# Optimization experiments

Hardware: AMD Instinct MI355X
Metric: run time of the kernel (lower is better)

## Reference

```python
import jax, jax.numpy as jnp
import numpy as np


def setup_inputs() -> dict:
    key = jax.random.key(0)
    k1, k2, k3, k4 = jax.random.split(key, 4)
    N, E, F_IN, F_OUT = 50000, 800000, 128, 128
    x = jax.random.normal(k1, (N, F_IN), dtype=jnp.float32)
    src = jax.random.randint(k2, (E,), 0, N, dtype=jnp.int32)
    dst = jax.random.randint(k3, (E,), 0, N, dtype=jnp.int32)
    # Linear(2*in, out, bias=False) weight, torch layout (out, 2*in)
    W = jax.random.normal(k4, (F_OUT, 2 * F_IN), dtype=jnp.float32) * (1.0 / np.sqrt(2 * F_IN))
    return {"x": x, "src": src, "dst": dst, "num_nodes": N, "W": W}


def reference(x, src, dst, num_nodes, W):
    # Mean aggregation over sparse adjacency (edge list src -> dst):
    # aggregated[v] = mean_{u in N(v)} x[u]
    msgs = x[src]                                            # [E, F] gather
    summed = jax.ops.segment_sum(msgs, dst, num_segments=num_nodes)  # [N, F]
    deg = jax.ops.segment_sum(jnp.ones_like(dst, dtype=x.dtype), dst,
                              num_segments=num_nodes)        # [N]
    agg = summed / jnp.maximum(deg, 1.0)[:, None]            # mean, safe for isolated nodes
    h = jnp.concatenate([x, agg], axis=1)                    # [N, 2F]
    out = h @ W.T                                            # [N, F_out]
    return jax.nn.relu(out)
```

## Files before the change

### kernel.cpp

```cpp
#include <hip/hip_runtime.h>
#include <hip/hip_bf16.h>

typedef __attribute__((ext_vector_type(8))) short short8;
typedef __attribute__((ext_vector_type(4))) float f32x4;

#define BKS      6
#define BKN      64
#define ITERA    16
#define NBMAX    1024
#define CAPB_MAX 3072

__device__ __forceinline__ unsigned short f2bf(float f) {
    unsigned u = __builtin_bit_cast(unsigned, f);
    u += 0x7fffu + ((u >> 16) & 1u);
    return (unsigned short)(u >> 16);
}
__device__ __forceinline__ float bf2f(unsigned short b) {
    return __builtin_bit_cast(float, ((unsigned)b) << 16);
}

__global__ void prep_kernel(const float* __restrict__ x,
                            unsigned short* __restrict__ xb,
                            const float* __restrict__ W,
                            unsigned short* __restrict__ Wp,
                            unsigned* __restrict__ gcur, int nb, int nx8) {
    int i = blockIdx.x * blockDim.x + threadIdx.x;
    if (i < nx8) {
        const float4* p = (const float4*)(x + (size_t)i * 8);
        float4 lo = p[0], hi = p[1];
        short8 v;
        v[0] = (short)f2bf(lo.x); v[1] = (short)f2bf(lo.y);
        v[2] = (short)f2bf(lo.z); v[3] = (short)f2bf(lo.w);
        v[4] = (short)f2bf(hi.x); v[5] = (short)f2bf(hi.y);
        v[6] = (short)f2bf(hi.z); v[7] = (short)f2bf(hi.w);
        *(short8*)(xb + (size_t)i * 8) = v;
    }
    if (i < 4096) {
        const float4* p = (const float4*)(W + (size_t)i * 8);
        float4 lo = p[0], hi = p[1];
        short8 v;
        v[0] = (short)f2bf(lo.x); v[1] = (short)f2bf(lo.y);
        v[2] = (short)f2bf(lo.z); v[3] = (short)f2bf(lo.w);
        v[4] = (short)f2bf(hi.x); v[5] = (short)f2bf(hi.y);
        v[6] = (short)f2bf(hi.z); v[7] = (short)f2bf(hi.w);
        int r    = i >> 5;
        int c0   = (i & 31) << 3;
        int ct   = r >> 4;
        int arow = r & 15;
        int ks   = c0 >> 5;
        int kgrp = (c0 >> 3) & 3;
        int l    = arow | (kgrp << 4);
        *(short8*)(Wp + (((size_t)(ct * 8 + ks) * 64 + l) * 8)) = v;
    }
    if (i < nb) gcur[i] = 0u;
}

__global__ __launch_bounds__(256) void bin_kernel(const int* __restrict__ src,
                                                  const int* __restrict__ dst,
                                                  unsigned* gcur,
                                                  unsigned* __restrict__ gbuf,
                                                  int E, int nb, int capb) {
    __shared__ unsigned cnt[NBMAX];
    __shared__ unsigned gbase[NBMAX];
    for (int t = threadIdx.x; t < nb; t += 256) cnt[t] = 0u;
    __syncthreads();

    int e0 = blockIdx.x * (256 * ITERA) + threadIdx.x;
    unsigned pk[ITERA];
    unsigned short bk[ITERA], pp[ITERA];
#pragma unroll
    for (int it = 0; it < ITERA; ++it) {
        int e = e0 + it * 256;
        bk[it] = 0xFFFFu;
        if (e < E) {
            int d = dst[e];
            unsigned b = (unsigned)d >> BKS;
            pk[it] = (unsigned)src[e] | ((unsigned)(d & (BKN - 1)) << 24);
            pp[it] = (unsigned short)atomicAdd(&cnt[b], 1u);
            bk[it] = (unsigned short)b;
        }
    }
    __syncthreads();
    for (int t = threadIdx.x; t < nb; t += 256)
        gbase[t] = cnt[t] ? atomicAdd(&gcur[t], cnt[t]) : 0u;
    __syncthreads();
#pragma unroll
    for (int it = 0; it < ITERA; ++it) {
        if (bk[it] != 0xFFFFu) {
            unsigned b = bk[it];
            unsigned off = gbase[b] + pp[it];
            if (off < (unsigned)capb) gbuf[(size_t)b * capb + off] = pk[it];
        }
    }
}

__global__ __launch_bounds__(512) void agg_gemm_kernel(
    const unsigned short* __restrict__ xb,
    const unsigned* __restrict__ gbuf,
    const unsigned* __restrict__ gcur,
    const unsigned short* __restrict__ Wp,
    float* __restrict__ out, int N, int capb)
{
    __shared__ unsigned cnt[BKN];
    __shared__ unsigned degs[BKN];
    __shared__ unsigned cur[BKN];
    __shared__ unsigned elist[CAPB_MAX];
    __shared__ unsigned short aggs[BKN][136];

    int tid = threadIdx.x;
    int b   = blockIdx.x;
    unsigned cntB = gcur[b];
    if (cntB > (unsigned)capb) cntB = (unsigned)capb;
    const unsigned* bb = gbuf + (size_t)b * capb;

    if (tid < BKN) cnt[tid] = 0u;
    __syncthreads();
    for (unsigned i = tid; i < cntB; i += 512)
        atomicAdd(&cnt[bb[i] >> 24], 1u);
    __syncthreads();
    if (tid < BKN) degs[tid] = cnt[tid];
    __syncthreads();
#pragma unroll
    for (int off = 1; off < BKN; off <<= 1) {
        unsigned t = (tid < BKN && tid >= off) ? cnt[tid - off] : 0u;
        __syncthreads();
        if (tid < BKN) cnt[tid] += t;
        __syncthreads();
    }
    if (tid < BKN) cur[tid] = cnt[tid] - degs[tid];
    __syncthreads();
    for (unsigned i = tid; i < cntB; i += 512) {
        unsigned pk = bb[i];
        unsigned p  = atomicAdd(&cur[pk >> 24], 1u);
        elist[p] = pk & 0x00FFFFFFu;
    }
    __syncthreads();

    int wv = tid >> 6, l = tid & 63;
    int q4 = l >> 4, ql = l & 15;
    int base = b << BKS;

    for (int r0 = wv; r0 < BKN; r0 += 8) {
        unsigned endi  = cnt[r0];
        unsigned dg    = degs[r0];
        unsigned start = endi - dg;
        float acc[8] = {0.f, 0.f, 0.f, 0.f, 0.f, 0.f, 0.f, 0.f};

        for (unsigned eb = start; eb < endi; eb += 16) {
            unsigned last = endi - 1;
            unsigned e0 = eb + q4, e1 = e0 + 4, e2 = e0 + 8, e3 = e0 + 12;
            float w0 = (e0 < endi) ? 1.0f : 0.0f;
            float w1 = (e1 < endi) ? 1.0f : 0.0f;
            float w2 = (e2 < endi) ? 1.0f : 0.0f;
            float w3 = (e3 < endi) ? 1.0f : 0.0f;
            unsigned i0 = (e0 < endi) ? e0 : last;
            unsigned i1 = (e1 < endi) ? e1 : last;
            unsigned i2 = (e2 < endi) ? e2 : last;
            unsigned i3 = (e3 < endi) ? e3 : last;
            unsigned s0 = elist[i0], s1 = elist[i1];
            unsigned s2 = elist[i2], s3 = elist[i3];
            short8 v0 = *(const short8*)(xb + (size_t)s0 * 128 + ql * 8);
            short8 v1 = *(const short8*)(xb + (size_t)s1 * 128 + ql * 8);
            short8 v2 = *(const short8*)(xb + (size_t)s2 * 128 + ql * 8);
            short8 v3 = *(const short8*)(xb + (size_t)s3 * 128 + ql * 8);
#pragma unroll
            for (int j = 0; j < 8; ++j) {
                acc[j] = fmaf(w0, bf2f((unsigned short)v0[j]), acc[j]);
                acc[j] = fmaf(w1, bf2f((unsigned short)v1[j]), acc[j]);
                acc[j] = fmaf(w2, bf2f((unsigned short)v2[j]), acc[j]);
                acc[j] = fmaf(w3, bf2f((unsigned short)v3[j]), acc[j]);
            }
        }

#pragma unroll
        for (int j = 0; j < 8; ++j) {
            acc[j] += __shfl_xor(acc[j], 16);
            acc[j] += __shfl_xor(acc[j], 32);
        }
        if (q4 == 0) {
            float inv = dg ? 1.0f / (float)dg : 1.0f;
            short8 st;
#pragma unroll
            for (int j = 0; j < 8; ++j) st[j] = (short)f2bf(acc[j] * inv);
            *(short8*)&aggs[r0][ql * 8] = st;
        }
    }
    __syncthreads();

    int w    = tid >> 6;
    int rt   = w >> 1;
    int cth  = w & 1;
    int arow = l & 15;
    int kgrp = l >> 4;
    int row  = base + rt * 16 + arow;
    bool rok = row < N;

    short8 afrag[8];
#pragma unroll
    for (int ks = 0; ks < 4; ++ks) {
        short8 a = {};
        if (rok) a = *(const short8*)(xb + (size_t)row * 128 + ks * 32 + kgrp * 8);
        afrag[ks] = a;
    }
#pragma unroll
    for (int ks = 0; ks < 4; ++ks)
        afrag[4 + ks] = *(const short8*)&aggs[rt * 16 + arow][ks * 32 + kgrp * 8];

    f32x4 acc[4];
#pragma unroll
    for (int c = 0; c < 4; ++c) acc[c] = (f32x4){0.f, 0.f, 0.f, 0.f};

#pragma unroll
    for (int ks = 0; ks < 8; ++ks) {
        short8 a = afrag[ks];
#pragma unroll
        for (int c = 0; c < 4; ++c) {
            int ct = cth * 4 + c;
            const short8* bp =
                (const short8*)(Wp + (((size_t)(ct * 8 + ks) * 64 + l) * 8));
            acc[c] = __builtin_amdgcn_mfma_f32_16x16x32_bf16(a, *bp, acc[c], 0, 0, 0);
        }
    }

#pragma unroll
    for (int c = 0; c < 4; ++c) {
#pragma unroll
        for (int r = 0; r < 4; ++r) {
            int orow = base + rt * 16 + kgrp * 4 + r;
            if (orow < N) {
                out[(size_t)orow * 128 + (cth * 4 + c) * 16 + arow] =
                    fmaxf(acc[c][r], 0.0f);
            }
        }
    }
}

extern "C" void kernel_launch(void* const* d_in, const int* in_sizes, int n_in,
                              void* d_out, int out_size, void* d_ws, size_t ws_size,
                              hipStream_t stream) {
    const float* x  = (const float*)d_in[0];
    const int* src  = (const int*)d_in[1];
    const int* dst  = (const int*)d_in[2];
    const float* W  = (const float*)d_in[4];

    int N = in_sizes[0] / 128;
    int E = in_sizes[1];
    float* out = (float*)d_out;

    int nb = (N + BKN - 1) >> BKS;
    int capb = 2 * (E / (nb > 0 ? nb : 1)) + 1024;
    capb = (capb + 63) & ~63;
    if (capb > CAPB_MAX) capb = CAPB_MAX;

    char* ws = (char*)d_ws;
    size_t o = 0;
    auto carve = [&](size_t bytes) {
        char* p = ws + o;
        o += (bytes + 255) & ~(size_t)255;
        return p;
    };
    unsigned* gcur     = (unsigned*)carve((size_t)nb * 4);
    unsigned* gbuf     = (unsigned*)carve((size_t)nb * capb * 4);
    unsigned short* Wp = (unsigned short*)carve(128 * 256 * 2);
    unsigned short* xb = (unsigned short*)carve((size_t)N * 128 * 2);
    (void)ws_size;

    int nx8 = N * 16;
    int pt  = nx8 > 4096 ? nx8 : 4096;
    if (pt < nb) pt = nb;

    prep_kernel<<<(pt + 255) / 256, 256, 0, stream>>>(x, xb, W, Wp, gcur, nb, nx8);
    bin_kernel<<<(E + 256 * ITERA - 1) / (256 * ITERA), 256, 0, stream>>>(
        src, dst, gcur, gbuf, E, nb, capb);
    agg_gemm_kernel<<<nb, 512, 0, stream>>>(xb, gbuf, gcur, Wp, out, N, capb);
}
```

Measured before the change: 74.80 us.

## Fuse prep and binning kernels; assign one aggregation row per quarter-wave

Merges the bf16 conversion kernel and the edge-binning kernel into one launch, and zeroes the global bucket counters with a memset issued beforehand. In the aggregation phase each 16-lane quarter-wave now owns its own destination row and walks its edges four at a time, so the cross-quarter shuffle reduction goes away. This cuts one launch and the shuffle traffic, but low-degree rows now leave more lanes idle and more loop iterations run serially per row. The conversion grid is sized by nx8, so binning runs only on the first blocks alongside it.

```diff
diff --git a/kernel.cpp b/kernel.cpp
--- a/kernel.cpp
+++ b/kernel.cpp
@@ -19,13 +19,20 @@
     return __builtin_bit_cast(float, ((unsigned)b) << 16);
 }
 
-__global__ void prep_kernel(const float* __restrict__ x,
-                            unsigned short* __restrict__ xb,
-                            const float* __restrict__ W,
-                            unsigned short* __restrict__ Wp,
-                            unsigned* __restrict__ gcur, int nb, int nx8) {
-    int i = blockIdx.x * blockDim.x + threadIdx.x;
-    if (i < nx8) {
+__global__ __launch_bounds__(256) void prepbin_kernel(
+    const float* __restrict__ x, unsigned short* __restrict__ xb,
+    const float* __restrict__ W, unsigned short* __restrict__ Wp,
+    const int* __restrict__ src, const int* __restrict__ dst,
+    unsigned* gcur, unsigned* __restrict__ gbuf,
+    int E, int nb, int capb, int nx8)
+{
+    __shared__ unsigned cnt[NBMAX];
+    __shared__ unsigned gbase[NBMAX];
+    int tid = threadIdx.x;
+    int gid = blockIdx.x * 256 + tid;
+    int gstr = gridDim.x * 256;
+
+    for (int i = gid; i < nx8; i += gstr) {
         const float4* p = (const float4*)(x + (size_t)i * 8);
         float4 lo = p[0], hi = p[1];
         short8 v;
@@ -35,16 +42,16 @@
         v[6] = (short)f2bf(hi.z); v[7] = (short)f2bf(hi.w);
         *(short8*)(xb + (size_t)i * 8) = v;
     }
-    if (i < 4096) {
-        const float4* p = (const float4*)(W + (size_t)i * 8);
+    if (gid < 4096) {
+        const float4* p = (const float4*)(W + (size_t)gid * 8);
         float4 lo = p[0], hi = p[1];
         short8 v;
         v[0] = (short)f2bf(lo.x); v[1] = (short)f2bf(lo.y);
         v[2] = (short)f2bf(lo.z); v[3] = (short)f2bf(lo.w);
         v[4] = (short)f2bf(hi.x); v[5] = (short)f2bf(hi.y);
         v[6] = (short)f2bf(hi.z); v[7] = (short)f2bf(hi.w);
-        int r    = i >> 5;
-        int c0   = (i & 31) << 3;
+        int r    = gid >> 5;
+        int c0   = (gid & 31) << 3;
         int ct   = r >> 4;
         int arow = r & 15;
         int ks   = c0 >> 5;
@@ -52,44 +59,38 @@
         int l    = arow | (kgrp << 4);
         *(short8*)(Wp + (((size_t)(ct * 8 + ks) * 64 + l) * 8)) = v;
     }
-    if (i < nb) gcur[i] = 0u;
-}
-
-__global__ __launch_bounds__(256) void bin_kernel(const int* __restrict__ src,
-                                                  const int* __restrict__ dst,
-                                                  unsigned* gcur,
-                                                  unsigned* __restrict__ gbuf,
-                                                  int E, int nb, int capb) {
-    __shared__ unsigned cnt[NBMAX];
-    __shared__ unsigned gbase[NBMAX];
-    for (int t = threadIdx.x; t < nb; t += 256) cnt[t] = 0u;
-    __syncthreads();
-
-    int e0 = blockIdx.x * (256 * ITERA) + threadIdx.x;
-    unsigned pk[ITERA];
-    unsigned short bk[ITERA], pp[ITERA];
-#pragma unroll
-    for (int it = 0; it < ITERA; ++it) {
-        int e = e0 + it * 256;
-        bk[it] = 0xFFFFu;
-        if (e < E) {
-            int d = dst[e];
-            unsigned b = (unsigned)d >> BKS;
-            pk[it] = (unsigned)src[e] | ((unsigned)(d & (BKN - 1)) << 24);
-            pp[it] = (unsigned short)atomicAdd(&cnt[b], 1u);
-            bk[it] = (unsigned short)b;
-        }
-    }
-    __syncthreads();
-    for (int t = threadIdx.x; t < nb; t += 256)
-        gbase[t] = cnt[t] ? atomicAdd(&gcur[t], cnt[t]) : 0u;
-    __syncthreads();
-#pragma unroll
-    for (int it = 0; it < ITERA; ++it) {
-        if (bk[it] != 0xFFFFu) {
-            unsigned b = bk[it];
-            unsigned off = gbase[b] + pp[it];
-            if (off < (unsigned)capb) gbuf[(size_t)b * capb + off] = pk[it];
+
+    int EB = (E + 256 * ITERA - 1) / (256 * ITERA);
+    if (blockIdx.x < EB) {
+        for (int t = tid; t < nb; t += 256) cnt[t] = 0u;
+        __syncthreads();
+
+        int e0 = blockIdx.x * (256 * ITERA) + tid;
+        unsigned pk[ITERA];
+        unsigned short bk[ITERA], pp[ITERA];
+#pragma unroll
+        for (int it = 0; it < ITERA; ++it) {
+            int e = e0 + it * 256;
+            bk[it] = 0xFFFFu;
+            if (e < E) {
+                int d = dst[e];
+                unsigned b = (unsigned)d >> BKS;
+                pk[it] = (unsigned)src[e] | ((unsigned)(d & (BKN - 1)) << 24);
+                pp[it] = (unsigned short)atomicAdd(&cnt[b], 1u);
+                bk[it] = (unsigned short)b;
+            }
+        }
+        __syncthreads();
+        for (int t = tid; t < nb; t += 256)
+            gbase[t] = cnt[t] ? atomicAdd(&gcur[t], cnt[t]) : 0u;
+        __syncthreads();
+#pragma unroll
+        for (int it = 0; it < ITERA; ++it) {
+            if (bk[it] != 0xFFFFu) {
+                unsigned b = bk[it];
+                unsigned off = gbase[b] + pp[it];
+                if (off < (unsigned)capb) gbuf[(size_t)b * capb + off] = pk[it];
+            }
         }
     }
 }
@@ -140,24 +141,25 @@
     int q4 = l >> 4, ql = l & 15;
     int base = b << BKS;
 
-    for (int r0 = wv; r0 < BKN; r0 += 8) {
+#pragma unroll
+    for (int pass = 0; pass < BKN / 32; ++pass) {
+        int r0 = pass * 32 + wv * 4 + q4;
         unsigned endi  = cnt[r0];
         unsigned dg    = degs[r0];
         unsigned start = endi - dg;
         float acc[8] = {0.f, 0.f, 0.f, 0.f, 0.f, 0.f, 0.f, 0.f};
 
-        for (unsigned eb = start; eb < endi; eb += 16) {
+        for (unsigned eb = start; eb < endi; eb += 4) {
             unsigned last = endi - 1;
-            unsigned e0 = eb + q4, e1 = e0 + 4, e2 = e0 + 8, e3 = e0 + 12;
-            float w0 = (e0 < endi) ? 1.0f : 0.0f;
+            unsigned e0 = eb, e1 = eb + 1, e2 = eb + 2, e3 = eb + 3;
+            float w0 = 1.0f;
             float w1 = (e1 < endi) ? 1.0f : 0.0f;
             float w2 = (e2 < endi) ? 1.0f : 0.0f;
             float w3 = (e3 < endi) ? 1.0f : 0.0f;
-            unsigned i0 = (e0 < endi) ? e0 : last;
             unsigned i1 = (e1 < endi) ? e1 : last;
             unsigned i2 = (e2 < endi) ? e2 : last;
             unsigned i3 = (e3 < endi) ? e3 : last;
-            unsigned s0 = elist[i0], s1 = elist[i1];
+            unsigned s0 = elist[e0], s1 = elist[i1];
             unsigned s2 = elist[i2], s3 = elist[i3];
             short8 v0 = *(const short8*)(xb + (size_t)s0 * 128 + ql * 8);
             short8 v1 = *(const short8*)(xb + (size_t)s1 * 128 + ql * 8);
@@ -172,18 +174,11 @@
             }
         }
 
-#pragma unroll
-        for (int j = 0; j < 8; ++j) {
-            acc[j] += __shfl_xor(acc[j], 16);
-            acc[j] += __shfl_xor(acc[j], 32);
-        }
-        if (q4 == 0) {
-            float inv = dg ? 1.0f / (float)dg : 1.0f;
-            short8 st;
-#pragma unroll
-            for (int j = 0; j < 8; ++j) st[j] = (short)f2bf(acc[j] * inv);
-            *(short8*)&aggs[r0][ql * 8] = st;
-        }
+        float inv = dg ? 1.0f / (float)dg : 1.0f;
+        short8 st;
+#pragma unroll
+        for (int j = 0; j < 8; ++j) st[j] = (short)f2bf(acc[j] * inv);
+        *(short8*)&aggs[r0][ql * 8] = st;
     }
     __syncthreads();
 
@@ -266,11 +261,13 @@
     (void)ws_size;
 
     int nx8 = N * 16;
-    int pt  = nx8 > 4096 ? nx8 : 4096;
-    if (pt < nb) pt = nb;
-
-    prep_kernel<<<(pt + 255) / 256, 256, 0, stream>>>(x, xb, W, Wp, gcur, nb, nx8);
-    bin_kernel<<<(E + 256 * ITERA - 1) / (256 * ITERA), 256, 0, stream>>>(
-        src, dst, gcur, gbuf, E, nb, capb);
+    int gb  = (nx8 + 255) / 256;
+    int eb  = (E + 256 * ITERA - 1) / (256 * ITERA);
+    if (gb < eb) gb = eb;
+    if (gb < 16) gb = 16;
+
+    hipMemsetAsync(gcur, 0, (size_t)nb * 4, stream);
+    prepbin_kernel<<<gb, 256, 0, stream>>>(x, xb, W, Wp, src, dst, gcur, gbuf,
+                                           E, nb, capb, nx8);
     agg_gemm_kernel<<<nb, 512, 0, stream>>>(xb, gbuf, gcur, Wp, out, N, capb);
 }
```

After: 74.06 us. No clear change (-1.0%).
